# Performance work log

Hardware: AMD Instinct MI355X
Metric: run time of the kernel (lower is better)

Reference implementation:

```python
import jax, jax.numpy as jnp
import numpy as np

D, C, H, W = 8, 512, 64, 64


def setup_inputs() -> dict:
    key = jax.random.key(0)
    k1, k2, k3 = jax.random.split(key, 3)
    x = jax.random.normal(k1, (D, C, H, W), dtype=jnp.float32)
    atten = jax.random.normal(k2, (D, C, C), dtype=jnp.float32)
    gamma = jax.random.normal(k3, (1,), dtype=jnp.float32)
    return {"x": x, "atten": atten, "gamma": gamma}


def reference(x, atten, gamma):
    d, c, h, w = x.shape
    q = x.reshape(d, c, h * w)              # q == v == flattened x; k = q^T
    # energy[d, i, j] = <channel_i, channel_j> over spatial positions
    energy = jnp.einsum('din,djn->dij', q, q)
    # max-centering: rowmax - energy (note the sign flip vs standard softmax)
    energy_new = jnp.max(energy, axis=-1, keepdims=True) - energy
    attention = jax.nn.softmax(energy_new, axis=-1)
    attention = jax.nn.softmax(attention + atten, axis=-1)
    # out = attention^T @ v : out[d, j, n] = sum_i attention[d, i, j] * v[d, i, n]
    out = jnp.einsum('dij,din->djn', attention, q).reshape(d, c, h, w)
    return gamma * out + x
```

## Files before the change

kernel.cpp:

```cpp
#include <hip/hip_runtime.h>
#include <hip/hip_bf16.h>

#define DD 8
#define CC 512
#define NN 4096

typedef __bf16 bf16x8 __attribute__((ext_vector_type(8)));
typedef float  f32x4  __attribute__((ext_vector_type(4)));
typedef ushort ush8   __attribute__((ext_vector_type(8)));

__device__ __forceinline__ ushort f2bf(float f) {
  unsigned u = __float_as_uint(f);
  u = (u + 0x7fffu + ((u >> 16) & 1u)) >> 16;
  return (ushort)u;
}
__device__ __forceinline__ float bf2f(ushort h) {
  return __uint_as_float(((unsigned)h) << 16);
}

__device__ __forceinline__ void gl_lds16(const ushort* g, ushort* l) {
  __builtin_amdgcn_global_load_lds(
      (const __attribute__((address_space(1))) void*)g,
      (__attribute__((address_space(3))) void*)l, 16, 0, 0);
}


__global__ __launch_bounds__(256) void k0_convert(
    const float* __restrict__ x, ushort* __restrict__ qh,
    ushort* __restrict__ ql, ushort* __restrict__ qt) {
  int d = blockIdx.z, ct = blockIdx.y, nt = blockIdx.x;
  __shared__ ushort T[64][68];
  int t = threadIdx.x;
  int rr = t >> 4;
  int c4 = (t & 15) * 4;
  const float* xb = x + ((size_t)(d * CC + ct * 64)) * NN + nt * 64;
#pragma unroll
  for (int it = 0; it < 4; ++it) {
    int r = it * 16 + rr;
    float4 v = *(const float4*)(xb + (size_t)r * NN + c4);
    ushort h0 = f2bf(v.x), h1 = f2bf(v.y), h2 = f2bf(v.z), h3 = f2bf(v.w);
    ushort l0 = f2bf(v.x - bf2f(h0)), l1 = f2bf(v.y - bf2f(h1));
    ushort l2 = f2bf(v.z - bf2f(h2)), l3 = f2bf(v.w - bf2f(h3));
    size_t qi = ((size_t)(d * CC + ct * 64 + r)) * NN + nt * 64 + c4;
    *(ushort4*)(qh + qi) = make_ushort4(h0, h1, h2, h3);
    *(ushort4*)(ql + qi) = make_ushort4(l0, l1, l2, l3);
    *(ushort4*)&T[r][c4] = make_ushort4(h0, h1, h2, h3);
  }
  __syncthreads();
#pragma unroll
  for (int it = 0; it < 4; ++it) {
    int nl = it * 16 + rr;
    ushort4 v = make_ushort4(T[c4 + 0][nl], T[c4 + 1][nl], T[c4 + 2][nl], T[c4 + 3][nl]);
    *(ushort4*)(qt + ((size_t)(d * NN + nt * 64 + nl)) * CC + ct * 64 + c4) = v;
  }
}

#define K1_STAGE(S)                                                            \
  {                                                                            \
    ushort* ls = lbase + ((S) & 1) * 8192;                                     \
    const ushort* gs = gsrc + (size_t)(S) * 32;                                \
    _Pragma("unroll")                                                          \
    for (int c = 0; c < 8; ++c)                                                \
      gl_lds16(gs + (size_t)c * 16 * NN, ls + c * 512);                        \
  }

#define K1_COMPUTE(SOFF)                                                       \
  {                                                                            \
    bf16x8 ah[4], al[4];                                                       \
    _Pragma("unroll")                                                          \
    for (int mi = 0; mi < 4; ++mi) {                                           \
      int off = (SOFF) + (wm + mi * 16 + fr) * 32 + qo;                        \
      ah[mi] = *(const bf16x8*)&As[off];                                       \
      al[mi] = *(const bf16x8*)&As[off + 4096];                                \
    }                                                                          \
    _Pragma("unroll")                                                          \
    for (int ni = 0; ni < 4; ++ni) {                                           \
      int off = (SOFF) + (wn + ni * 16 + fr) * 32 + qo;                        \
      bf16x8 bh = *(const bf16x8*)&Bs[off];                                    \
      bf16x8 bl = *(const bf16x8*)&Bs[off + 4096];                             \
      _Pragma("unroll")                                                        \
      for (int mi = 0; mi < 4; ++mi) {                                         \
        acc[mi][ni] = __builtin_amdgcn_mfma_f32_16x16x32_bf16(ah[mi], bh, acc[mi][ni], 0, 0, 0); \
        acc[mi][ni] = __builtin_amdgcn_mfma_f32_16x16x32_bf16(ah[mi], bl, acc[mi][ni], 0, 0, 0); \
        acc[mi][ni] = __builtin_amdgcn_mfma_f32_16x16x32_bf16(al[mi], bh, acc[mi][ni], 0, 0, 0); \
      }                                                                        \
    }                                                                          \
  }

__global__ __launch_bounds__(256, 2) void k1_gram(
    const ushort* __restrict__ qh, const ushort* __restrict__ ql,
    float* __restrict__ Ep, int ns, int nkk, int ksp) {
  __shared__ ushort As[2 * 2 * 4096];
  __shared__ ushort Bs[2 * 2 * 4096];
  int b = blockIdx.x;
  int s = b % ns;
  int rem = b / ns;
  int tile = rem % 10, d = rem / 10;
  int tm = (int)((0x3221110000ULL >> (tile * 4)) & 15ULL);
  int tn = (int)((0x3323213210ULL >> (tile * 4)) & 15ULL);
  int t = threadIdx.x, lane = t & 63, w = t >> 6;
  int wm = (w >> 1) * 64, wn = (w & 1) * 64;
  int qd = lane >> 4, fr = lane & 15;
  int qo = (qd ^ ((fr >> 1) & 3)) * 8;
  int so = ((lane & 3) ^ ((lane >> 3) & 3)) * 8;

  const ushort* srcbase = (w & 1) ? ql : qh;
  int rowblk = (w < 2) ? tm : tn;
  const ushort* gsrc = srcbase +
      ((size_t)(d * CC + rowblk * 128 + (lane >> 2))) * NN +
      (size_t)s * ksp + so;
  ushort* lbase = ((w < 2) ? As : Bs) + (w & 1) * 4096;

  f32x4 acc[4][4];
#pragma unroll
  for (int i = 0; i < 4; ++i)
#pragma unroll
    for (int j = 0; j < 4; ++j) acc[i][j] = (f32x4){0.f, 0.f, 0.f, 0.f};

  K1_STAGE(0)

#pragma unroll 1
  for (int kk = 0; kk < nkk - 1; ++kk) {
    asm volatile("s_waitcnt lgkmcnt(0)\n\ts_barrier" ::: "memory");
    K1_STAGE(kk + 1)
    asm volatile("s_waitcnt vmcnt(8)\n\ts_barrier" ::: "memory");
    K1_COMPUTE((kk & 1) * 8192)
  }
  asm volatile("s_waitcnt vmcnt(0) lgkmcnt(0)\n\ts_barrier" ::: "memory");
  K1_COMPUTE(((nkk - 1) & 1) * 8192)

  size_t ebase = ((size_t)(s * DD + d)) * ((size_t)CC * CC);
#pragma unroll
  for (int mi = 0; mi < 4; ++mi) {
    int r0 = tm * 128 + wm + mi * 16 + qd * 4;
#pragma unroll
    for (int ni = 0; ni < 4; ++ni) {
      int c0 = tn * 128 + wn + ni * 16 + fr;
      float* ep = Ep + ebase + (size_t)r0 * CC + c0;
#pragma unroll
      for (int r = 0; r < 4; ++r) ep[(size_t)r * CC] = acc[mi][ni][r];
    }
  }
  if (tm != tn) {
#pragma unroll
    for (int mi = 0; mi < 4; ++mi) {
      int r0 = tm * 128 + wm + mi * 16 + qd * 4;
#pragma unroll
      for (int ni = 0; ni < 4; ++ni) {
        int c0 = tn * 128 + wn + ni * 16 + fr;
        float4 v = make_float4(acc[mi][ni][0], acc[mi][ni][1],
                               acc[mi][ni][2], acc[mi][ni][3]);
        *(float4*)(Ep + ebase + (size_t)c0 * CC + r0) = v;
      }
    }
  }
}

__device__ __forceinline__ float wmin(float v) {
#pragma unroll
  for (int o = 32; o > 0; o >>= 1) v = fminf(v, __shfl_xor(v, o));
  return v;
}
__device__ __forceinline__ float wmax(float v) {
#pragma unroll
  for (int o = 32; o > 0; o >>= 1) v = fmaxf(v, __shfl_xor(v, o));
  return v;
}
__device__ __forceinline__ float wsum(float v) {
#pragma unroll
  for (int o = 32; o > 0; o >>= 1) v += __shfl_xor(v, o);
  return v;
}

__global__ __launch_bounds__(256) void k2_softmax(
    const float* __restrict__ Ep, const float* __restrict__ atten,
    ushort* __restrict__ a2t, int ns) {
  int d = blockIdx.x & 7;
  int i0 = (blockIdx.x >> 3) * 8;
  int t = threadIdx.x, lane = t & 63, w = t >> 6;
  int j8 = lane * 8;
  __shared__ ushort T[8][520];
  const size_t SP = (size_t)DD * CC * CC;

#pragma unroll
  for (int r2 = 0; r2 < 2; ++r2) {
    int ri = w * 2 + r2;
    size_t base = ((size_t)(d * CC + i0 + ri)) * CC + j8;
    f32x4 a0 = (f32x4){0.f, 0.f, 0.f, 0.f};
    f32x4 a1 = (f32x4){0.f, 0.f, 0.f, 0.f};
    for (int s = 0; s < ns; ++s) {
      const float* p = Ep + (size_t)s * SP + base;
      a0 += *(const f32x4*)p;
      a1 += *(const f32x4*)(p + 4);
    }
    float mn = fminf(fminf(fminf(a0[0], a0[1]), fminf(a0[2], a0[3])),
                     fminf(fminf(a1[0], a1[1]), fminf(a1[2], a1[3])));
    mn = wmin(mn);
    float p0 = __expf(mn - a0[0]), p1 = __expf(mn - a0[1]);
    float p2 = __expf(mn - a0[2]), p3 = __expf(mn - a0[3]);
    float p4 = __expf(mn - a1[0]), p5 = __expf(mn - a1[1]);
    float p6 = __expf(mn - a1[2]), p7 = __expf(mn - a1[3]);
    float s1 = wsum(p0 + p1 + p2 + p3 + p4 + p5 + p6 + p7);
    float inv1 = 1.0f / s1;
    const float* ap = atten + base;
    f32x4 t0 = *(const f32x4*)ap;
    f32x4 t1 = *(const f32x4*)(ap + 4);
    float u0 = p0 * inv1 + t0[0], u1 = p1 * inv1 + t0[1];
    float u2 = p2 * inv1 + t0[2], u3 = p3 * inv1 + t0[3];
    float u4 = p4 * inv1 + t1[0], u5 = p5 * inv1 + t1[1];
    float u6 = p6 * inv1 + t1[2], u7 = p7 * inv1 + t1[3];
    float mx = wmax(fmaxf(fmaxf(fmaxf(u0, u1), fmaxf(u2, u3)),
                          fmaxf(fmaxf(u4, u5), fmaxf(u6, u7))));
    float q0 = __expf(u0 - mx), q1 = __expf(u1 - mx);
    float q2 = __expf(u2 - mx), q3 = __expf(u3 - mx);
    float q4 = __expf(u4 - mx), q5 = __expf(u5 - mx);
    float q6 = __expf(u6 - mx), q7 = __expf(u7 - mx);
    float s2 = wsum(q0 + q1 + q2 + q3 + q4 + q5 + q6 + q7);
    float inv2 = 1.0f / s2;
    ush8 o;
    o[0] = f2bf(q0 * inv2); o[1] = f2bf(q1 * inv2);
    o[2] = f2bf(q2 * inv2); o[3] = f2bf(q3 * inv2);
    o[4] = f2bf(q4 * inv2); o[5] = f2bf(q5 * inv2);
    o[6] = f2bf(q6 * inv2); o[7] = f2bf(q7 * inv2);
    *(ush8*)&T[ri][j8] = o;
  }
  __syncthreads();
#pragma unroll
  for (int it = 0; it < 2; ++it) {
    int j = t + it * 256;
    ush8 o;
#pragma unroll
    for (int k = 0; k < 8; ++k) o[k] = T[k][j];
    *(ush8*)&a2t[((size_t)(d * CC + j)) * CC + i0] = o;
  }
}

#define K3_STAGE(S)                                                            \
  {                                                                            \
    ushort* ls = lds0 + ((S) % 3) * stsz;                                      \
    const ushort* gs = g0 + (size_t)(S) * 32;                                  \
    _Pragma("unroll")                                                          \
    for (int c = 0; c < 4; ++c)                                                \
      gl_lds16(gs + (size_t)(c * 16) * CC, ls + c * 512);                      \
    if (!isA) {                                                                \
      _Pragma("unroll")                                                        \
      for (int c = 4; c < 8; ++c)                                              \
        gl_lds16(gs + (size_t)(c * 16) * CC, ls + c * 512);                    \
    }                                                                          \
  }

#define K3_COMPUTE(S)                                                          \
  {                                                                            \
    int soA = ((S) % 3) * 4096, soB = ((S) % 3) * 8192;                        \
    bf16x8 qf[8];                                                              \
    _Pragma("unroll")                                                          \
    for (int ii = 0; ii < 8; ++ii)                                             \
      qf[ii] = *(const bf16x8*)&Bs[soB + (wn2 + ii * 16 + fr) * 32 + qo];      \
    _Pragma("unroll")                                                          \
    for (int jj = 0; jj < 4; ++jj) {                                           \
      bf16x8 af = *(const bf16x8*)&As[soA + (wj + jj * 16 + fr) * 32 + qo];    \
      _Pragma("unroll")                                                        \
      for (int ii = 0; ii < 8; ++ii)                                           \
        acc[ii][jj] = __builtin_amdgcn_mfma_f32_16x16x32_bf16(                 \
            qf[ii], af, acc[ii][jj], 0, 0, 0);                                 \
    }                                                                          \
  }

#define K3_WAIT                                                                \
  {                                                                            \
    if (isA) asm volatile("s_waitcnt vmcnt(4)" ::: "memory");                  \
    else     asm volatile("s_waitcnt vmcnt(8)" ::: "memory");                  \
    asm volatile("s_barrier" ::: "memory");                                    \
  }

__global__ __launch_bounds__(256, 2) void k3_out(
    const ushort* __restrict__ a2t, const ushort* __restrict__ qt,
    const float* __restrict__ x, const float* __restrict__ gamma,
    float* __restrict__ out) {
  __shared__ ushort As[3 * 4096];
  __shared__ ushort Bs[3 * 8192];
  int b = blockIdx.x;
  int d = b & 7, jt = (b >> 3) & 3, ntp = b >> 5;
  int t = threadIdx.x, lane = t & 63, w = t >> 6;
  int wj = (w >> 1) * 64;
  int wn2 = (w & 1) * 128;
  int qd = lane >> 4, fr = lane & 15;
  int qo = (qd ^ ((fr >> 1) & 3)) * 8;
  int so = ((lane & 3) ^ ((lane >> 3) & 3)) * 8;

  int isA = (w < 2);
  const ushort* src = isA
      ? (a2t + (size_t)d * CC * CC + (size_t)(jt * 128) * CC)
      : (qt + (size_t)d * NN * CC + (size_t)(ntp * 256) * CC);
  int rbase = (w & 1) * (isA ? 64 : 128);
  const ushort* g0 = src + ((size_t)(rbase + (lane >> 2))) * CC + so;
  ushort* lds0 = (isA ? As : Bs) + rbase * 32;
  int stsz = isA ? 4096 : 8192;

  f32x4 acc[8][4];
#pragma unroll
  for (int i = 0; i < 8; ++i)
#pragma unroll
    for (int j = 0; j < 4; ++j) acc[i][j] = (f32x4){0.f, 0.f, 0.f, 0.f};

  K3_STAGE(0)
  K3_STAGE(1)

#pragma unroll 1
  for (int kk = 0; kk < 14; ++kk) {
    K3_WAIT
    K3_STAGE(kk + 2)
    K3_COMPUTE(kk)
  }
  K3_WAIT
  K3_COMPUTE(14)
  asm volatile("s_waitcnt vmcnt(0)" ::: "memory");
  asm volatile("s_barrier" ::: "memory");

  float g = gamma[0];
  int n0b = ntp * 256 + wn2 + qd * 4;
  int jb = jt * 128 + wj + fr;
  float4 xp[4], xq[4];
#pragma unroll
  for (int jj = 0; jj < 4; ++jj) {
    size_t rb = ((size_t)(d * CC + jb + jj * 16)) * NN;
    xp[jj] = *(const float4*)(x + rb + n0b);
    xq[jj] = *(const float4*)(x + rb + n0b + 16);
  }
  K3_COMPUTE(15)

#pragma unroll
  for (int ii = 0; ii < 8; ++ii) {
    float4 xn[4];
    if (ii < 6) {
#pragma unroll
      for (int jj = 0; jj < 4; ++jj)
        xn[jj] = *(const float4*)(x + ((size_t)(d * CC + jb + jj * 16)) * NN +
                                  n0b + (ii + 2) * 16);
    }
#pragma unroll
    for (int jj = 0; jj < 4; ++jj) {
      size_t idx = ((size_t)(d * CC + jb + jj * 16)) * NN + n0b + ii * 16;
      *(float4*)(out + idx) = make_float4(g * acc[ii][jj][0] + xp[jj].x,
                                          g * acc[ii][jj][1] + xp[jj].y,
                                          g * acc[ii][jj][2] + xp[jj].z,
                                          g * acc[ii][jj][3] + xp[jj].w);
    }
    if (ii < 6) {
#pragma unroll
      for (int jj = 0; jj < 4; ++jj) { xp[jj] = xq[jj]; xq[jj] = xn[jj]; }
    } else if (ii == 6) {
#pragma unroll
      for (int jj = 0; jj < 4; ++jj) xp[jj] = xq[jj];
    }
  }
}

extern "C" void kernel_launch(void* const* d_in, const int* in_sizes, int n_in,
                              void* d_out, int out_size, void* d_ws, size_t ws_size,
                              hipStream_t stream) {
  (void)in_sizes; (void)n_in; (void)out_size;
  const float* x     = (const float*)d_in[0];
  const float* atten = (const float*)d_in[1];
  const float* gamma = (const float*)d_in[2];
  float* out = (float*)d_out;

  char* ws = (char*)d_ws;
  ushort* qh  = (ushort*)(ws);
  ushort* ql  = (ushort*)(ws + 33554432);
  ushort* qt  = (ushort*)(ws + 67108864);
  ushort* a2t = (ushort*)(ws + 100663296);
  float*  Ep  = (float*) (ws + 104857600);

  int ns = (ws_size >= 104857600ULL + 8ULL * 8388608ULL) ? 8 : 4;
  int ksp = NN / ns;
  int nkk = ksp / 32;

  k0_convert<<<dim3(64, 8, 8), 256, 0, stream>>>(x, qh, ql, qt);
  k1_gram   <<<dim3(80 * ns), 256, 0, stream>>>(qh, ql, Ep, ns, nkk, ksp);
  k2_softmax<<<dim3(512), 256, 0, stream>>>(Ep, atten, a2t, ns);
  k3_out    <<<dim3(512), 256, 0, stream>>>(a2t, qt, x, gamma, out);
}
```

Before: 237.0 us.

## Enlarge k3 output tile to 256x256 with 512-thread blocks

The output GEMM kernel now uses 512-thread blocks computing a 256(j) x 256(n) tile, with 256 blocks instead of 512. Each wave still computes 64x128 and loads one equal-sized slice of A or B per stage, which balances the global-to-LDS loads and removes the isA branching in staging and waiting. The larger tile halves how often qt is re-read across j-tiles. In exchange, LDS use per block doubles to 96KB, which may limit residency to one block per CU, and the grid is smaller.

New measurement: 231.0 us. -2.6%, faster.

```diff
diff --git a/kernel.cpp b/kernel.cpp
--- a/kernel.cpp
+++ b/kernel.cpp
@@ -237,50 +237,39 @@
 
 #define K3_STAGE(S)                                                            \
   {                                                                            \
-    ushort* ls = lds0 + ((S) % 3) * stsz;                                      \
+    ushort* ls = lds0 + ((S) % 3) * 8192;                                      \
     const ushort* gs = g0 + (size_t)(S) * 32;                                  \
     _Pragma("unroll")                                                          \
     for (int c = 0; c < 4; ++c)                                                \
       gl_lds16(gs + (size_t)(c * 16) * CC, ls + c * 512);                      \
-    if (!isA) {                                                                \
-      _Pragma("unroll")                                                        \
-      for (int c = 4; c < 8; ++c)                                              \
-        gl_lds16(gs + (size_t)(c * 16) * CC, ls + c * 512);                    \
-    }                                                                          \
   }
 
 #define K3_COMPUTE(S)                                                          \
   {                                                                            \
-    int soA = ((S) % 3) * 4096, soB = ((S) % 3) * 8192;                        \
-    bf16x8 qf[8];                                                              \
+    int soff = ((S) % 3) * 8192;                                               \
+    bf16x8 qf[8], af[4];                                                       \
     _Pragma("unroll")                                                          \
     for (int ii = 0; ii < 8; ++ii)                                             \
-      qf[ii] = *(const bf16x8*)&Bs[soB + (wn2 + ii * 16 + fr) * 32 + qo];      \
-    _Pragma("unroll")                                                          \
-    for (int jj = 0; jj < 4; ++jj) {                                           \
-      bf16x8 af = *(const bf16x8*)&As[soA + (wj + jj * 16 + fr) * 32 + qo];    \
+      qf[ii] = *(const bf16x8*)&Bs[soff + (wn2 + ii * 16 + fr) * 32 + qo];     \
+    _Pragma("unroll")                                                          \
+    for (int jj = 0; jj < 4; ++jj)                                             \
+      af[jj] = *(const bf16x8*)&As[soff + (wj + jj * 16 + fr) * 32 + qo];      \
+    _Pragma("unroll")                                                          \
+    for (int jj = 0; jj < 4; ++jj)                                             \
       _Pragma("unroll")                                                        \
       for (int ii = 0; ii < 8; ++ii)                                           \
         acc[ii][jj] = __builtin_amdgcn_mfma_f32_16x16x32_bf16(                 \
-            qf[ii], af, acc[ii][jj], 0, 0, 0);                                 \
-    }                                                                          \
-  }
-
-#define K3_WAIT                                                                \
-  {                                                                            \
-    if (isA) asm volatile("s_waitcnt vmcnt(4)" ::: "memory");                  \
-    else     asm volatile("s_waitcnt vmcnt(8)" ::: "memory");                  \
-    asm volatile("s_barrier" ::: "memory");                                    \
-  }
-
-__global__ __launch_bounds__(256, 2) void k3_out(
+            qf[ii], af[jj], acc[ii][jj], 0, 0, 0);                             \
+  }
+
+__global__ __launch_bounds__(512, 2) void k3_out(
     const ushort* __restrict__ a2t, const ushort* __restrict__ qt,
     const float* __restrict__ x, const float* __restrict__ gamma,
     float* __restrict__ out) {
-  __shared__ ushort As[3 * 4096];
+  __shared__ ushort As[3 * 8192];
   __shared__ ushort Bs[3 * 8192];
   int b = blockIdx.x;
-  int d = b & 7, jt = (b >> 3) & 3, ntp = b >> 5;
+  int d = b & 7, jt = (b >> 3) & 1, ntp = b >> 4;
   int t = threadIdx.x, lane = t & 63, w = t >> 6;
   int wj = (w >> 1) * 64;
   int wn2 = (w & 1) * 128;
@@ -288,14 +277,13 @@
   int qo = (qd ^ ((fr >> 1) & 3)) * 8;
   int so = ((lane & 3) ^ ((lane >> 3) & 3)) * 8;
 
-  int isA = (w < 2);
+  int isA = (w < 4);
+  int rbase = (w & 3) * 64;
   const ushort* src = isA
-      ? (a2t + (size_t)d * CC * CC + (size_t)(jt * 128) * CC)
+      ? (a2t + (size_t)d * CC * CC + (size_t)(jt * 256) * CC)
       : (qt + (size_t)d * NN * CC + (size_t)(ntp * 256) * CC);
-  int rbase = (w & 1) * (isA ? 64 : 128);
   const ushort* g0 = src + ((size_t)(rbase + (lane >> 2))) * CC + so;
   ushort* lds0 = (isA ? As : Bs) + rbase * 32;
-  int stsz = isA ? 4096 : 8192;
 
   f32x4 acc[8][4];
 #pragma unroll
@@ -308,18 +296,18 @@
 
 #pragma unroll 1
   for (int kk = 0; kk < 14; ++kk) {
-    K3_WAIT
+    asm volatile("s_waitcnt vmcnt(4)\n\ts_barrier" ::: "memory");
     K3_STAGE(kk + 2)
     K3_COMPUTE(kk)
   }
-  K3_WAIT
+  asm volatile("s_waitcnt vmcnt(4)\n\ts_barrier" ::: "memory");
   K3_COMPUTE(14)
   asm volatile("s_waitcnt vmcnt(0)" ::: "memory");
   asm volatile("s_barrier" ::: "memory");
 
   float g = gamma[0];
   int n0b = ntp * 256 + wn2 + qd * 4;
-  int jb = jt * 128 + wj + fr;
+  int jb = jt * 256 + wj + fr;
   float4 xp[4], xq[4];
 #pragma unroll
   for (int jj = 0; jj < 4; ++jj) {
@@ -379,5 +367,5 @@
   k0_convert<<<dim3(64, 8, 8), 256, 0, stream>>>(x, qh, ql, qt);
   k1_gram   <<<dim3(80 * ns), 256, 0, stream>>>(qh, ql, Ep, ns, nkk, ksp);
   k2_softmax<<<dim3(512), 256, 0, stream>>>(Ep, atten, a2t, ns);
-  k3_out    <<<dim3(512), 256, 0, stream>>>(a2t, qt, x, gamma, out);
-}
+  k3_out    <<<dim3(256), 512, 0, stream>>>(a2t, qt, x, gamma, out);
+}
```
